# Performance work log

Hardware: AMD Instinct MI355X
Metric: run time of the kernel (lower is better)

## Reference

```python
import jax, jax.numpy as jnp
import numpy as np

N = 8192      # total nodes
B = 8         # graphs in batch
L = 1024      # nodes per graph (max_len)
E = 262144    # edges (before self loops)
IN = 64       # in_channels
H = 8         # heads
C = 32        # hidden_channels (per-head out dim)
D = H * C     # 256, d_model
DFF = 2048    # transformer FFN dim (torch default)
NEG = -1e9


def setup_inputs() -> dict:
    key = jax.random.key(0)
    ks = jax.random.split(key, 24)
    def p(i, shape):
        return jax.random.normal(ks[i], shape, jnp.float32) * 0.02
    x = jax.random.normal(ks[0], (N, IN), jnp.float32)
    src = jax.random.randint(ks[1], (E,), 0, N)
    dst = (src // L) * L + jax.random.randint(ks[2], (E,), 0, L)  # keep edges within a graph
    edge_index = jnp.stack([src, dst]).astype(jnp.int32)
    batch = (jnp.arange(N) // L).astype(jnp.int32)
    return dict(
        x=x, edge_index=edge_index, batch=batch,
        gat_W0=p(3, (D, IN)), gat_W12=p(4, (2, D, D)),
        gat_att_src=p(5, (3, H, C)), gat_att_dst=p(6, (3, H, C)), gat_bias=p(7, (3, D)),
        tf_qkv_w=p(8, (2, 3 * D, D)), tf_qkv_b=p(9, (2, 3 * D)),
        tf_out_w=p(10, (2, D, D)), tf_out_b=p(11, (2, D)),
        tf_ln1_w=jnp.ones((2, D)), tf_ln1_b=jnp.zeros((2, D)),
        tf_ln2_w=jnp.ones((2, D)), tf_ln2_b=jnp.zeros((2, D)),
        tf_ff1_w=p(12, (2, DFF, D)), tf_ff1_b=p(13, (2, DFF)),
        tf_ff2_w=p(14, (2, D, DFF)), tf_ff2_b=p(15, (2, D)),
        pred_w=p(16, (3, D)), pred_b=p(17, (3,)),
    )


def _gat(x, src, dst, W, att_s, att_d, bias):
    # PyG GATConv, concat=True, add_self_loops (appended in caller), eval (no dropout)
    h = (x @ W.T).reshape(-1, H, C)                       # [N,H,C]
    a_s = (h * att_s).sum(-1)                             # [N,H]
    a_d = (h * att_d).sum(-1)
    e = jax.nn.leaky_relu(a_s[src] + a_d[dst], 0.2)       # [E+N,H]
    m = jax.ops.segment_max(e, dst, num_segments=N)       # per-dst softmax
    e = jnp.exp(e - m[dst])
    s = jax.ops.segment_sum(e, dst, num_segments=N)
    alpha = e / s[dst]
    out = jax.ops.segment_sum(h[src] * alpha[..., None], dst, num_segments=N)
    return out.reshape(-1, D) + bias


def _ln(x, w, b):
    mu = x.mean(-1, keepdims=True)
    v = ((x - mu) ** 2).mean(-1, keepdims=True)
    return (x - mu) / jnp.sqrt(v + 1e-5) * w + b


def _tf_layer(x, mask, qkv_w, qkv_b, out_w, out_b, ln1w, ln1b, ln2w, ln2b, f1w, f1b, f2w, f2b):
    # torch TransformerEncoderLayer (post-LN, relu), key padding mask, eval mode
    qkv = x @ qkv_w.T + qkv_b                              # [B,L,3D]
    q, k, v = jnp.split(qkv, 3, -1)
    sh = lambda t: t.reshape(B, L, H, D // H)
    q, k, v = sh(q), sh(k), sh(v)
    sc = jnp.einsum('bqhd,bkhd->bhqk', q, k) * (1.0 / float(np.sqrt(D // H)))
    sc = jnp.where(mask[:, None, None, :], NEG, sc)
    a = jax.nn.softmax(sc, -1)
    o = jnp.einsum('bhqk,bkhd->bqhd', a, v).reshape(B, L, D)
    x = _ln(x + o @ out_w.T + out_b, ln1w, ln1b)
    f = jax.nn.relu(x @ f1w.T + f1b) @ f2w.T + f2b
    return _ln(x + f, ln2w, ln2b)


def reference(x, edge_index, batch, gat_W0, gat_W12, gat_att_src, gat_att_dst, gat_bias,
              tf_qkv_w, tf_qkv_b, tf_out_w, tf_out_b, tf_ln1_w, tf_ln1_b, tf_ln2_w, tf_ln2_b,
              tf_ff1_w, tf_ff1_b, tf_ff2_w, tf_ff2_b, pred_w, pred_b):
    loops = jnp.arange(N, dtype=edge_index.dtype)
    src = jnp.concatenate([edge_index[0], loops])
    dst = jnp.concatenate([edge_index[1], loops])
    h = jax.nn.relu(_gat(x, src, dst, gat_W0, gat_att_src[0], gat_att_dst[0], gat_bias[0]))
    for i in range(2):
        h = jax.nn.relu(_gat(h, src, dst, gat_W12[i], gat_att_src[i + 1], gat_att_dst[i + 1], gat_bias[i + 1]))
    # ragged -> padded [B, L, D] (vectorized scatter instead of python loop)
    seq_lens = jax.ops.segment_sum(jnp.ones(N, jnp.int32), batch, num_segments=B)
    starts = jnp.cumsum(seq_lens) - seq_lens
    pos = jnp.arange(N) - starts[batch]
    xp = jnp.zeros((B, L, D), h.dtype).at[batch, pos].set(h)
    mask = jnp.arange(L)[None, :] >= seq_lens[:, None]     # True = padded key
    for i in range(2):
        xp = _tf_layer(xp, mask, tf_qkv_w[i], tf_qkv_b[i], tf_out_w[i], tf_out_b[i],
                       tf_ln1_w[i], tf_ln1_b[i], tf_ln2_w[i], tf_ln2_b[i],
                       tf_ff1_w[i], tf_ff1_b[i], tf_ff2_w[i], tf_ff2_b[i])
    return xp @ pred_w.T + pred_b                          # [B,L,3]
```

## Files before the change

kernel.cpp:

```cpp
#include <hip/hip_runtime.h>
#include <hip/hip_bf16.h>

#define NN 8192
#define EE 262144
#define BB 8
#define LL 1024
#define HH 8
#define DD 256
#define DFFN 2048

typedef short s8v __attribute__((ext_vector_type(8)));
typedef float f32x4 __attribute__((ext_vector_type(4)));
typedef unsigned short ushort;

__device__ inline ushort f2bf(float f) {
    unsigned u = __float_as_uint(f);
    u = (u + 0x7fffu + ((u >> 16) & 1u)) >> 16;
    return (ushort)u;
}
__device__ inline float bf2f(ushort u) {
    return __uint_as_float(((unsigned)u) << 16);
}

template<bool BIAS, bool RELU, bool RES, bool WF, bool WB>
__global__ __launch_bounds__(256) void mgemm_kernel(
    const ushort* __restrict__ A, const ushort* __restrict__ W,
    const float* __restrict__ bias, const float* __restrict__ res,
    float* __restrict__ Cf, ushort* __restrict__ Cb, int M, int N, int K)
{
    __shared__ ushort As[128 * 64];
    __shared__ ushort Bs[128 * 64];
    int t = threadIdx.x;
    int l = t & 63;
    int quad = l >> 4, l15 = l & 15;
    int r7 = l15 & 7;
    int w = t >> 6;
    int wm = (w >> 1) * 64, wn = (w & 1) * 64;
    int m0 = blockIdx.x * 128, n0 = blockIdx.y * 128;

    f32x4 z = {0.f, 0.f, 0.f, 0.f};
    f32x4 acc[4][4];
#pragma unroll
    for (int i = 0; i < 4; ++i)
#pragma unroll
        for (int j = 0; j < 4; ++j) acc[i][j] = z;

    for (int k0 = 0; k0 < K; k0 += 64) {
#pragma unroll
        for (int i = 0; i < 4; ++i) {
            int chunk = i * 256 + t;
            int r = chunk >> 3, p = chunk & 7;
            int qs = (p ^ (r & 7)) * 8;
            __builtin_amdgcn_global_load_lds(
                (const __attribute__((address_space(1))) unsigned int*)
                    (A + (size_t)(m0 + r) * K + k0 + qs),
                (__attribute__((address_space(3))) unsigned int*)(As + chunk * 8), 16, 0, 0);
            __builtin_amdgcn_global_load_lds(
                (const __attribute__((address_space(1))) unsigned int*)
                    (W + (size_t)(n0 + r) * K + k0 + qs),
                (__attribute__((address_space(3))) unsigned int*)(Bs + chunk * 8), 16, 0, 0);
        }
        __syncthreads();
#pragma unroll
        for (int kk = 0; kk < 2; ++kk) {
            int off = ((kk * 4 + quad) ^ r7) * 8;
            s8v af[4], bfv[4];
#pragma unroll
            for (int i = 0; i < 4; ++i) {
                af[i]  = *(const s8v*)(As + (wm + i * 16 + l15) * 64 + off);
                bfv[i] = *(const s8v*)(Bs + (wn + i * 16 + l15) * 64 + off);
            }
#pragma unroll
            for (int mi = 0; mi < 4; ++mi)
#pragma unroll
                for (int ni = 0; ni < 4; ++ni)
                    acc[mi][ni] = __builtin_amdgcn_mfma_f32_16x16x32_bf16(
                        af[mi], bfv[ni], acc[mi][ni], 0, 0, 0);
        }
        __syncthreads();
    }

#pragma unroll
    for (int mi = 0; mi < 4; ++mi) {
#pragma unroll
        for (int ni = 0; ni < 4; ++ni) {
            int n = n0 + wn + ni * 16 + l15;
#pragma unroll
            for (int r = 0; r < 4; ++r) {
                int m = m0 + wm + mi * 16 + quad * 4 + r;
                float v = acc[mi][ni][r];
                if (BIAS) v += bias[n];
                if (RES)  v += res[(size_t)m * N + n];
                if (RELU) v = fmaxf(v, 0.f);
                if (WF) Cf[(size_t)m * N + n] = v;
                if (WB) Cb[(size_t)m * N + n] = f2bf(v);
            }
        }
    }
}

template<bool ASD>
__global__ __launch_bounds__(256) void mgemm64_kernel(
    const ushort* __restrict__ A, const ushort* __restrict__ W,
    ushort* __restrict__ Cb,
    const float* __restrict__ atts, const float* __restrict__ attd,
    float* __restrict__ a_s, float* __restrict__ a_d, int M, int N, int K)
{
    __shared__ ushort As[64 * 64];
    __shared__ ushort Bs[64 * 64];
    int t = threadIdx.x;
    int l = t & 63;
    int quad = l >> 4, l15 = l & 15;
    int r7 = l15 & 7;
    int w = t >> 6;
    int wm = (w >> 1) * 32, wn = (w & 1) * 32;
    int m0 = blockIdx.x * 64, n0 = blockIdx.y * 64;

    f32x4 z = {0.f, 0.f, 0.f, 0.f};
    f32x4 acc[2][2];
#pragma unroll
    for (int i = 0; i < 2; ++i)
#pragma unroll
        for (int j = 0; j < 2; ++j) acc[i][j] = z;

    for (int k0 = 0; k0 < K; k0 += 64) {
#pragma unroll
        for (int i = 0; i < 2; ++i) {
            int chunk = i * 256 + t;
            int r = chunk >> 3, p = chunk & 7;
            int qs = (p ^ (r & 7)) * 8;
            __builtin_amdgcn_global_load_lds(
                (const __attribute__((address_space(1))) unsigned int*)
                    (A + (size_t)(m0 + r) * K + k0 + qs),
                (__attribute__((address_space(3))) unsigned int*)(As + chunk * 8), 16, 0, 0);
            __builtin_amdgcn_global_load_lds(
                (const __attribute__((address_space(1))) unsigned int*)
                    (W + (size_t)(n0 + r) * K + k0 + qs),
                (__attribute__((address_space(3))) unsigned int*)(Bs + chunk * 8), 16, 0, 0);
        }
        __syncthreads();
#pragma unroll
        for (int kk = 0; kk < 2; ++kk) {
            s8v af[2], bfv[2];
            int off = ((kk * 4 + quad) ^ r7) * 8;
#pragma unroll
            for (int i = 0; i < 2; ++i) {
                af[i]  = *(const s8v*)(As + (wm + i * 16 + l15) * 64 + off);
                bfv[i] = *(const s8v*)(Bs + (wn + i * 16 + l15) * 64 + off);
            }
#pragma unroll
            for (int mi = 0; mi < 2; ++mi)
#pragma unroll
                for (int ni = 0; ni < 2; ++ni)
                    acc[mi][ni] = __builtin_amdgcn_mfma_f32_16x16x32_bf16(
                        af[mi], bfv[ni], acc[mi][ni], 0, 0, 0);
        }
        __syncthreads();
    }

#pragma unroll
    for (int mi = 0; mi < 2; ++mi) {
#pragma unroll
        for (int ni = 0; ni < 2; ++ni) {
            int n = n0 + wn + ni * 16 + l15;
#pragma unroll
            for (int r = 0; r < 4; ++r) {
                int m = m0 + wm + mi * 16 + quad * 4 + r;
                Cb[(size_t)m * N + n] = f2bf(acc[mi][ni][r]);
            }
        }
    }

    if (ASD) {
        int head = ((n0 + wn) >> 5) & 7;
        float as0 = atts[head * 32 + l15];
        float as1 = atts[head * 32 + 16 + l15];
        float ad0 = attd[head * 32 + l15];
        float ad1 = attd[head * 32 + 16 + l15];
#pragma unroll
        for (int mi = 0; mi < 2; ++mi)
#pragma unroll
            for (int r = 0; r < 4; ++r) {
                float sp = acc[mi][0][r] * as0 + acc[mi][1][r] * as1;
                float dp = acc[mi][0][r] * ad0 + acc[mi][1][r] * ad1;
#pragma unroll
                for (int off = 1; off < 16; off <<= 1) {
                    sp += __shfl_xor(sp, off);
                    dp += __shfl_xor(dp, off);
                }
                if (l15 == 0) {
                    int m = m0 + wm + mi * 16 + quad * 4 + r;
                    a_s[m * 8 + head] = sp;
                    a_d[m * 8 + head] = dp;
                }
            }
    }
}

__global__ __launch_bounds__(256) void gemm0_scatter_kernel(
    const ushort* __restrict__ A, const ushort* __restrict__ W,
    ushort* __restrict__ Cb,
    const float* __restrict__ atts, const float* __restrict__ attd,
    float* __restrict__ a_s, float* __restrict__ a_d,
    const int* __restrict__ ei, int* __restrict__ deg, int* __restrict__ col)
{
    __shared__ ushort As[64 * 64];
    __shared__ ushort Bs[64 * 64];
    int t = threadIdx.x;

    if (blockIdx.x >= 512) {
        int e = (blockIdx.x - 512) * 256 + t;
        if (e < EE + NN) {
            int s, d;
            if (e < EE) { s = ei[e]; d = ei[EE + e]; } else { s = e - EE; d = s; }
            int slot = atomicAdd(&deg[d], 1);
            col[(d << 7) + slot] = s;
        }
        return;
    }

    int l = t & 63;
    int quad = l >> 4, l15 = l & 15;
    int r7 = l15 & 7;
    int w = t >> 6;
    int wm = (w >> 1) * 32, wn = (w & 1) * 32;
    int m0 = (blockIdx.x & 127) * 64, n0 = (blockIdx.x >> 7) * 64;
    const int K = 64;

    f32x4 z = {0.f, 0.f, 0.f, 0.f};
    f32x4 acc[2][2];
#pragma unroll
    for (int i = 0; i < 2; ++i)
#pragma unroll
        for (int j = 0; j < 2; ++j) acc[i][j] = z;

#pragma unroll
    for (int i = 0; i < 2; ++i) {
        int chunk = i * 256 + t;
        int r = chunk >> 3, p = chunk & 7;
        int qs = (p ^ (r & 7)) * 8;
        __builtin_amdgcn_global_load_lds(
            (const __attribute__((address_space(1))) unsigned int*)
                (A + (size_t)(m0 + r) * K + qs),
            (__attribute__((address_space(3))) unsigned int*)(As + chunk * 8), 16, 0, 0);
        __builtin_amdgcn_global_load_lds(
            (const __attribute__((address_space(1))) unsigned int*)
                (W + (size_t)(n0 + r) * K + qs),
            (__attribute__((address_space(3))) unsigned int*)(Bs + chunk * 8), 16, 0, 0);
    }
    __syncthreads();
#pragma unroll
    for (int kk = 0; kk < 2; ++kk) {
        s8v af[2], bfv[2];
        int off = ((kk * 4 + quad) ^ r7) * 8;
#pragma unroll
        for (int i = 0; i < 2; ++i) {
            af[i]  = *(const s8v*)(As + (wm + i * 16 + l15) * 64 + off);
            bfv[i] = *(const s8v*)(Bs + (wn + i * 16 + l15) * 64 + off);
        }
#pragma unroll
        for (int mi = 0; mi < 2; ++mi)
#pragma unroll
            for (int ni = 0; ni < 2; ++ni)
                acc[mi][ni] = __builtin_amdgcn_mfma_f32_16x16x32_bf16(
                    af[mi], bfv[ni], acc[mi][ni], 0, 0, 0);
    }

#pragma unroll
    for (int mi = 0; mi < 2; ++mi) {
#pragma unroll
        for (int ni = 0; ni < 2; ++ni) {
            int n = n0 + wn + ni * 16 + l15;
#pragma unroll
            for (int r = 0; r < 4; ++r) {
                int m = m0 + wm + mi * 16 + quad * 4 + r;
                Cb[(size_t)m * DD + n] = f2bf(acc[mi][ni][r]);
            }
        }
    }

    {
        int head = ((n0 + wn) >> 5) & 7;
        float as0 = atts[head * 32 + l15];
        float as1 = atts[head * 32 + 16 + l15];
        float ad0 = attd[head * 32 + l15];
        float ad1 = attd[head * 32 + 16 + l15];
#pragma unroll
        for (int mi = 0; mi < 2; ++mi)
#pragma unroll
            for (int r = 0; r < 4; ++r) {
                float sp = acc[mi][0][r] * as0 + acc[mi][1][r] * as1;
                float dp = acc[mi][0][r] * ad0 + acc[mi][1][r] * ad1;
#pragma unroll
                for (int off = 1; off < 16; off <<= 1) {
                    sp += __shfl_xor(sp, off);
                    dp += __shfl_xor(dp, off);
                }
                if (l15 == 0) {
                    int m = m0 + wm + mi * 16 + quad * 4 + r;
                    a_s[m * 8 + head] = sp;
                    a_d[m * 8 + head] = dp;
                }
            }
    }
}

template<bool PRED>
__global__ __launch_bounds__(256) void mgemm_ln_kernel(
    const ushort* __restrict__ A, const ushort* __restrict__ W,
    const float* __restrict__ bias, const float* __restrict__ res,
    const float* __restrict__ lnw, const float* __restrict__ lnbb,
    float* __restrict__ Xf, ushort* __restrict__ Xb,
    const float* __restrict__ pw, const float* __restrict__ pb,
    float* __restrict__ pout, int M, int K)
{
    __shared__ ushort As[16 * 64];
    __shared__ ushort Bs[256 * 64];
    __shared__ float red[2][4][16];
    __shared__ float predred[4][16][3];

    int t = threadIdx.x;
    int l = t & 63;
    int quad = l >> 4, l15 = l & 15;
    int r7 = l15 & 7;
    int w = t >> 6;
    int m0 = blockIdx.x * 16;
    int n0w = w * 64;

    f32x4 z = {0.f, 0.f, 0.f, 0.f};
    f32x4 acc[4];
#pragma unroll
    for (int i = 0; i < 4; ++i) acc[i] = z;

    for (int k0 = 0; k0 < K; k0 += 64) {
#pragma unroll
        for (int i = 0; i < 8; ++i) {
            int chunk = i * 256 + t;
            int r = chunk >> 3, p = chunk & 7;
            int qs = (p ^ (r & 7)) * 8;
            __builtin_amdgcn_global_load_lds(
                (const __attribute__((address_space(1))) unsigned int*)
                    (W + (size_t)r * K + k0 + qs),
                (__attribute__((address_space(3))) unsigned int*)(Bs + chunk * 8), 16, 0, 0);
        }
        if (t < 128) {
            int r = t >> 3, p = t & 7;
            int qs = (p ^ (r & 7)) * 8;
            __builtin_amdgcn_global_load_lds(
                (const __attribute__((address_space(1))) unsigned int*)
                    (A + (size_t)(m0 + r) * K + k0 + qs),
                (__attribute__((address_space(3))) unsigned int*)(As + t * 8), 16, 0, 0);
        }
        __syncthreads();
#pragma unroll
        for (int kk = 0; kk < 2; ++kk) {
            int off = ((kk * 4 + quad) ^ r7) * 8;
            s8v af = *(const s8v*)(As + l15 * 64 + off);
#pragma unroll
            for (int ni = 0; ni < 4; ++ni) {
                s8v bfv = *(const s8v*)(Bs + (n0w + ni * 16 + l15) * 64 + off);
                acc[ni] = __builtin_amdgcn_mfma_f32_16x16x32_bf16(af, bfv, acc[ni], 0, 0, 0);
            }
        }
        __syncthreads();
    }

    float v[4][4];
#pragma unroll
    for (int ni = 0; ni < 4; ++ni) {
        int n = n0w + ni * 16 + l15;
        float bi = bias[n];
#pragma unroll
        for (int r = 0; r < 4; ++r) {
            int m = m0 + quad * 4 + r;
            v[ni][r] = acc[ni][r] + bi + res[(size_t)m * DD + n];
        }
    }
    float s1[4], s2[4];
#pragma unroll
    for (int r = 0; r < 4; ++r) {
        s1[r] = 0.f; s2[r] = 0.f;
#pragma unroll
        for (int ni = 0; ni < 4; ++ni) { s1[r] += v[ni][r]; s2[r] += v[ni][r] * v[ni][r]; }
#pragma unroll
        for (int off = 1; off < 16; off <<= 1) {
            s1[r] += __shfl_xor(s1[r], off);
            s2[r] += __shfl_xor(s2[r], off);
        }
    }
    if (l15 == 0)
#pragma unroll
        for (int r = 0; r < 4; ++r) {
            red[0][w][quad * 4 + r] = s1[r];
            red[1][w][quad * 4 + r] = s2[r];
        }
    __syncthreads();
    float mu[4], rstd[4];
#pragma unroll
    for (int r = 0; r < 4; ++r) {
        int row = quad * 4 + r;
        float S1 = red[0][0][row] + red[0][1][row] + red[0][2][row] + red[0][3][row];
        float S2 = red[1][0][row] + red[1][1][row] + red[1][2][row] + red[1][3][row];
        mu[r] = S1 * (1.f / 256.f);
        float var = S2 * (1.f / 256.f) - mu[r] * mu[r];
        rstd[r] = rsqrtf(fmaxf(var, 0.f) + 1e-5f);
    }

    float ov[4][4];
#pragma unroll
    for (int ni = 0; ni < 4; ++ni) {
        int n = n0w + ni * 16 + l15;
        float wl = lnw[n], bl = lnbb[n];
#pragma unroll
        for (int r = 0; r < 4; ++r)
            ov[ni][r] = (v[ni][r] - mu[r]) * rstd[r] * wl + bl;
    }

    if (PRED) {
        float ps[3][4] = {};
#pragma unroll
        for (int ni = 0; ni < 4; ++ni) {
            int n = n0w + ni * 16 + l15;
            float w0 = pw[n], w1 = pw[DD + n], w2 = pw[2 * DD + n];
#pragma unroll
            for (int r = 0; r < 4; ++r) {
                ps[0][r] += ov[ni][r] * w0;
                ps[1][r] += ov[ni][r] * w1;
                ps[2][r] += ov[ni][r] * w2;
            }
        }
#pragma unroll
        for (int o3 = 0; o3 < 3; ++o3)
#pragma unroll
            for (int r = 0; r < 4; ++r)
#pragma unroll
                for (int off = 1; off < 16; off <<= 1)
                    ps[o3][r] += __shfl_xor(ps[o3][r], off);
        if (l15 == 0)
#pragma unroll
            for (int o3 = 0; o3 < 3; ++o3)
#pragma unroll
                for (int r = 0; r < 4; ++r)
                    predred[w][quad * 4 + r][o3] = ps[o3][r];
        __syncthreads();
        if (t < 48) {
            int row = t / 3, o3 = t % 3;
            float s = predred[0][row][o3] + predred[1][row][o3]
                    + predred[2][row][o3] + predred[3][row][o3] + pb[o3];
            pout[(size_t)(m0 + row) * 3 + o3] = s;
        }
    } else {
#pragma unroll
        for (int ni = 0; ni < 4; ++ni) {
            int n = n0w + ni * 16 + l15;
#pragma unroll
            for (int r = 0; r < 4; ++r) {
                int m = m0 + quad * 4 + r;
                Xf[(size_t)m * DD + n] = ov[ni][r];
                Xb[(size_t)m * DD + n] = f2bf(ov[ni][r]);
            }
        }
    }
}

__global__ __launch_bounds__(256) void mgemm_qkv_kernel(
    const ushort* __restrict__ A, const ushort* __restrict__ W,
    const float* __restrict__ bias,
    ushort* __restrict__ Qb, ushort* __restrict__ Kb, ushort* __restrict__ Vt,
    int M, int K)
{
    __shared__ ushort As[64 * 64];
    __shared__ ushort Bs[64 * 64];
    int t = threadIdx.x;
    int l = t & 63;
    int quad = l >> 4, l15 = l & 15;
    int r7 = l15 & 7;
    int w = t >> 6;
    int wm = (w >> 1) * 32, wn = (w & 1) * 32;
    int m0 = blockIdx.x * 64, n0 = blockIdx.y * 64;

    f32x4 z = {0.f, 0.f, 0.f, 0.f};
    f32x4 acc[2][2];
#pragma unroll
    for (int i = 0; i < 2; ++i)
#pragma unroll
        for (int j = 0; j < 2; ++j) acc[i][j] = z;

    for (int k0 = 0; k0 < K; k0 += 64) {
#pragma unroll
        for (int i = 0; i < 2; ++i) {
            int chunk = i * 256 + t;
            int r = chunk >> 3, p = chunk & 7;
            int qs = (p ^ (r & 7)) * 8;
            __builtin_amdgcn_global_load_lds(
                (const __attribute__((address_space(1))) unsigned int*)
                    (A + (size_t)(m0 + r) * K + k0 + qs),
                (__attribute__((address_space(3))) unsigned int*)(As + chunk * 8), 16, 0, 0);
            __builtin_amdgcn_global_load_lds(
                (const __attribute__((address_space(1))) unsigned int*)
                    (W + (size_t)(n0 + r) * K + k0 + qs),
                (__attribute__((address_space(3))) unsigned int*)(Bs + chunk * 8), 16, 0, 0);
        }
        __syncthreads();
#pragma unroll
        for (int kk = 0; kk < 2; ++kk) {
            s8v af[2], bfv[2];
            int off = ((kk * 4 + quad) ^ r7) * 8;
#pragma unroll
            for (int i = 0; i < 2; ++i) {
                af[i]  = *(const s8v*)(As + (wm + i * 16 + l15) * 64 + off);
                bfv[i] = *(const s8v*)(Bs + (wn + i * 16 + l15) * 64 + off);
            }
#pragma unroll
            for (int mi = 0; mi < 2; ++mi)
#pragma unroll
                for (int ni = 0; ni < 2; ++ni)
                    acc[mi][ni] = __builtin_amdgcn_mfma_f32_16x16x32_bf16(
                        af[mi], bfv[ni], acc[mi][ni], 0, 0, 0);
        }
        __syncthreads();
    }

#pragma unroll
    for (int mi = 0; mi < 2; ++mi) {
#pragma unroll
        for (int ni = 0; ni < 2; ++ni) {
            int n = n0 + wn + ni * 16 + l15;
            int sec = n >> 8, hc = n & 255;
            int hh = hc >> 5, c = hc & 31;
            float bv = bias[n];
#pragma unroll
            for (int r = 0; r < 4; ++r) {
                int m = m0 + wm + mi * 16 + quad * 4 + r;
                float v = acc[mi][ni][r] + bv;
                int b = m >> 10, ll2 = m & 1023;
                int bh = b * 8 + hh;
                if (sec == 0)
                    Qb[(size_t)bh * 32768 + ll2 * 32 + c] = f2bf(v * 0.17677669529663687f);
                else if (sec == 1)
                    Kb[(size_t)bh * 32768 + ll2 * 32 + c] = f2bf(v);
                else
                    Vt[(size_t)bh * 32768 + c * 1024 + ll2] = f2bf(v);
            }
        }
    }
}

__global__ __launch_bounds__(256) void castall_kernel(
    const float* __restrict__ W0, const float* __restrict__ W12,
    const float* __restrict__ qkvw, const float* __restrict__ outw,
    const float* __restrict__ f1w, const float* __restrict__ f2w,
    const float* __restrict__ x,
    ushort* __restrict__ W0b, ushort* __restrict__ W12b,
    ushort* __restrict__ qkvb, ushort* __restrict__ outb,
    ushort* __restrict__ f1b, ushort* __restrict__ f2b,
    ushort* __restrict__ xb, int* __restrict__ deg)
{
    int tid = blockIdx.x * 256 + threadIdx.x;
    if (tid < 2048) *(int4*)(deg + tid * 4) = make_int4(0, 0, 0, 0);
    int e = tid * 4;
    if (e >= 3293184) return;
    const float* s; ushort* d; int off;
    if (e < 16384)        { s = W0;   d = W0b;  off = e; }
    else if (e < 147456)  { s = W12;  d = W12b; off = e - 16384; }
    else if (e < 540672)  { s = qkvw; d = qkvb; off = e - 147456; }
    else if (e < 671744)  { s = outw; d = outb; off = e - 540672; }
    else if (e < 1720320) { s = f1w;  d = f1b;  off = e - 671744; }
    else if (e < 2768896) { s = f2w;  d = f2b;  off = e - 1720320; }
    else                  { s = x;    d = xb;   off = e - 2768896; }
    float4 v = *(const float4*)(s + off);
    d[off + 0] = f2bf(v.x); d[off + 1] = f2bf(v.y);
    d[off + 2] = f2bf(v.z); d[off + 3] = f2bf(v.w);
}

template<bool WF>
__global__ __launch_bounds__(256) void gat_agg_kernel(
    const ushort* __restrict__ hlinb, const float* __restrict__ a_s,
    const float* __restrict__ a_d, const int* __restrict__ deg,
    const int* __restrict__ col, const float* __restrict__ bias,
    float* __restrict__ out, ushort* __restrict__ outb)
{
    int wid = threadIdx.x >> 6, lane = threadIdx.x & 63;
    int dst = blockIdx.x * 4 + wid;
    int start = dst << 7;
    int end = start + deg[dst];
    int myh = lane >> 3;
    float adh = a_d[(size_t)dst * HH + myh];

    float a0 = 0.f, a1 = 0.f, a2 = 0.f, a3 = 0.f, den = 0.f;
    int e = start;
    for (; e + 4 <= end; e += 4) {
        int s0 = col[e], s1 = col[e + 1], s2 = col[e + 2], s3 = col[e + 3];
        float v0 = a_s[(size_t)s0 * HH + myh] + adh;
        float v1 = a_s[(size_t)s1 * HH + myh] + adh;
        float v2 = a_s[(size_t)s2 * HH + myh] + adh;
        float v3 = a_s[(size_t)s3 * HH + myh] + adh;
        v0 = v0 > 0.f ? v0 : 0.2f * v0;
        v1 = v1 > 0.f ? v1 : 0.2f * v1;
        v2 = v2 > 0.f ? v2 : 0.2f * v2;
        v3 = v3 > 0.f ? v3 : 0.2f * v3;
        float p0 = __expf(v0), p1 = __expf(v1), p2 = __expf(v2), p3 = __expf(v3);
        den += p0 + p1 + p2 + p3;
        uint2 h0 = *(const uint2*)(hlinb + (size_t)s0 * DD + lane * 4);
        uint2 h1 = *(const uint2*)(hlinb + (size_t)s1 * DD + lane * 4);
        uint2 h2 = *(const uint2*)(hlinb + (size_t)s2 * DD + lane * 4);
        uint2 h3 = *(const uint2*)(hlinb + (size_t)s3 * DD + lane * 4);
        a0 += p0 * bf2f((ushort)(h0.x & 0xffff)) + p1 * bf2f((ushort)(h1.x & 0xffff))
            + p2 * bf2f((ushort)(h2.x & 0xffff)) + p3 * bf2f((ushort)(h3.x & 0xffff));
        a1 += p0 * bf2f((ushort)(h0.x >> 16)) + p1 * bf2f((ushort)(h1.x >> 16))
            + p2 * bf2f((ushort)(h2.x >> 16)) + p3 * bf2f((ushort)(h3.x >> 16));
        a2 += p0 * bf2f((ushort)(h0.y & 0xffff)) + p1 * bf2f((ushort)(h1.y & 0xffff))
            + p2 * bf2f((ushort)(h2.y & 0xffff)) + p3 * bf2f((ushort)(h3.y & 0xffff));
        a3 += p0 * bf2f((ushort)(h0.y >> 16)) + p1 * bf2f((ushort)(h1.y >> 16))
            + p2 * bf2f((ushort)(h2.y >> 16)) + p3 * bf2f((ushort)(h3.y >> 16));
    }
    for (; e < end; ++e) {
        int s = col[e];
        float v = a_s[(size_t)s * HH + myh] + adh;
        v = v > 0.f ? v : 0.2f * v;
        float p = __expf(v);
        den += p;
        uint2 hv = *(const uint2*)(hlinb + (size_t)s * DD + lane * 4);
        a0 += p * bf2f((ushort)(hv.x & 0xffff));
        a1 += p * bf2f((ushort)(hv.x >> 16));
        a2 += p * bf2f((ushort)(hv.y & 0xffff));
        a3 += p * bf2f((ushort)(hv.y >> 16));
    }
    float inv = 1.f / den;
    float4 bv = *(const float4*)(bias + lane * 4);
    float r0 = fmaxf(a0 * inv + bv.x, 0.f);
    float r1 = fmaxf(a1 * inv + bv.y, 0.f);
    float r2 = fmaxf(a2 * inv + bv.z, 0.f);
    float r3 = fmaxf(a3 * inv + bv.w, 0.f);
    if (WF) {
        float* op = out + (size_t)dst * DD + lane * 4;
        op[0] = r0; op[1] = r1; op[2] = r2; op[3] = r3;
    }
    ushort* ob = outb + (size_t)dst * DD + lane * 4;
    ob[0] = f2bf(r0); ob[1] = f2bf(r1); ob[2] = f2bf(r2); ob[3] = f2bf(r3);
}

__global__ __launch_bounds__(256, 2) void attn_flash_kernel(
    const ushort* __restrict__ Qb, const ushort* __restrict__ Kb,
    const ushort* __restrict__ Vt, ushort* __restrict__ outb)
{
    __shared__ ushort Ks[2][128 * 32];
    __shared__ ushort Vs[2][32 * 128];
    __shared__ ushort pw[4][32][132];

    int t = threadIdx.x;
    int w = t >> 6, lane = t & 63;
    int quad = lane >> 4, l15 = lane & 15;
    int kq = (quad ^ ((l15 >> 1) & 3)) * 8;
    int bh = blockIdx.y;
    int q0 = blockIdx.x * 128 + w * 32;
    int b = bh >> 3, h = bh & 7;

    const ushort* qbase = Qb + (size_t)bh * 32768;
    const ushort* kbase = Kb + (size_t)bh * 32768;
    const ushort* vbase = Vt + (size_t)bh * 32768;

    s8v aq0 = *(const s8v*)(qbase + (q0 + l15) * 32 + quad * 8);
    s8v aq1 = *(const s8v*)(qbase + (q0 + 16 + l15) * 32 + quad * 8);

    int i0 = t, i1 = 256 + t;
    int kr0 = i0 >> 2, kcs0 = (((i0 & 3)) ^ ((kr0 >> 1) & 3)) * 8;
    int kr1 = i1 >> 2, kcs1 = (((i1 & 3)) ^ ((kr1 >> 1) & 3)) * 8;
    int vr0 = i0 >> 4, vcs0 = ((i0 & 15) ^ (vr0 & 15)) * 8;
    int vr1 = i1 >> 4, vcs1 = ((i1 & 15) ^ (vr1 & 15)) * 8;

#define STAGE(ch, bf)                                                          \
    {                                                                          \
        int j0 = (ch) * 128;                                                   \
        __builtin_amdgcn_global_load_lds(                                      \
            (const __attribute__((address_space(1))) unsigned int*)            \
                (kbase + (size_t)(j0 + kr0) * 32 + kcs0),                      \
            (__attribute__((address_space(3))) unsigned int*)(Ks[bf] + i0 * 8), 16, 0, 0); \
        __builtin_amdgcn_global_load_lds(                                      \
            (const __attribute__((address_space(1))) unsigned int*)            \
                (kbase + (size_t)(j0 + kr1) * 32 + kcs1),                      \
            (__attribute__((address_space(3))) unsigned int*)(Ks[bf] + i1 * 8), 16, 0, 0); \
        __builtin_amdgcn_global_load_lds(                                      \
            (const __attribute__((address_space(1))) unsigned int*)            \
                (vbase + (size_t)vr0 * 1024 + j0 + vcs0),                      \
            (__attribute__((address_space(3))) unsigned int*)(Vs[bf] + i0 * 8), 16, 0, 0); \
        __builtin_amdgcn_global_load_lds(                                      \
            (const __attribute__((address_space(1))) unsigned int*)            \
                (vbase + (size_t)vr1 * 1024 + j0 + vcs1),                      \
            (__attribute__((address_space(3))) unsigned int*)(Vs[bf] + i1 * 8), 16, 0, 0); \
    }

    f32x4 z = {0.f, 0.f, 0.f, 0.f};
    f32x4 o00 = z, o01 = z, o10 = z, o11 = z;
    float lden0[4] = {0.f, 0.f, 0.f, 0.f};
    float lden1[4] = {0.f, 0.f, 0.f, 0.f};

    STAGE(0, 0);
    for (int ch = 0; ch < 8; ++ch) {
        int bf = ch & 1;
        __syncthreads();
        if (ch < 7) STAGE(ch + 1, bf ^ 1);

        f32x4 s0[8], s1[8];
#pragma unroll
        for (int kk = 0; kk < 8; ++kk) {
            s8v bk = *(const s8v*)(Ks[bf] + (kk * 16 + l15) * 32 + kq);
            s0[kk] = __builtin_amdgcn_mfma_f32_16x16x32_bf16(aq0, bk, z, 0, 0, 0);
            s1[kk] = __builtin_amdgcn_mfma_f32_16x16x32_bf16(aq1, bk, z, 0, 0, 0);
        }

        float cs0[4] = {0.f, 0.f, 0.f, 0.f};
        float cs1[4] = {0.f, 0.f, 0.f, 0.f};
#pragma unroll
        for (int kk = 0; kk < 8; ++kk) {
#pragma unroll
            for (int r = 0; r < 4; ++r) {
                float p0 = __expf(s0[kk][r]);
                float p1 = __expf(s1[kk][r]);
                cs0[r] += p0;
                cs1[r] += p1;
                pw[w][quad * 4 + r][kk * 16 + l15]      = f2bf(p0);
                pw[w][16 + quad * 4 + r][kk * 16 + l15] = f2bf(p1);
            }
        }
#pragma unroll
        for (int r = 0; r < 4; ++r) {
#pragma unroll
            for (int off = 1; off < 16; off <<= 1) {
                cs0[r] += __shfl_xor(cs0[r], off);
                cs1[r] += __shfl_xor(cs1[r], off);
            }
            lden0[r] += cs0[r];
            lden1[r] += cs1[r];
        }

#pragma unroll
        for (int kk = 0; kk < 4; ++kk) {
            s8v ap0 = *(const s8v*)(&pw[w][l15][kk * 32 + quad * 8]);
            s8v ap1 = *(const s8v*)(&pw[w][16 + l15][kk * 32 + quad * 8]);
            int c0 = ((kk * 4 + quad) ^ l15) * 8;
            s8v b0 = *(const s8v*)(Vs[bf] + (size_t)l15 * 128 + c0);
            s8v b1 = *(const s8v*)(Vs[bf] + (size_t)(16 + l15) * 128 + c0);
            o00 = __builtin_amdgcn_mfma_f32_16x16x32_bf16(ap0, b0, o00, 0, 0, 0);
            o01 = __builtin_amdgcn_mfma_f32_16x16x32_bf16(ap0, b1, o01, 0, 0, 0);
            o10 = __builtin_amdgcn_mfma_f32_16x16x32_bf16(ap1, b0, o10, 0, 0, 0);
            o11 = __builtin_amdgcn_mfma_f32_16x16x32_bf16(ap1, b1, o11, 0, 0, 0);
        }
    }
#undef STAGE

#pragma unroll
    for (int r = 0; r < 4; ++r) {
        int row0 = q0 + quad * 4 + r;
        int row1 = row0 + 16;
        float i0v = 1.f / lden0[r];
        float i1v = 1.f / lden1[r];
        outb[(size_t)(b * 1024 + row0) * 256 + h * 32 + l15]      = f2bf(o00[r] * i0v);
        outb[(size_t)(b * 1024 + row0) * 256 + h * 32 + 16 + l15] = f2bf(o01[r] * i0v);
        outb[(size_t)(b * 1024 + row1) * 256 + h * 32 + l15]      = f2bf(o10[r] * i1v);
        outb[(size_t)(b * 1024 + row1) * 256 + h * 32 + 16 + l15] = f2bf(o11[r] * i1v);
    }
}

extern "C" void kernel_launch(void* const* d_in, const int* in_sizes, int n_in,
                              void* d_out, int out_size, void* d_ws, size_t ws_size,
                              hipStream_t stream)
{
    const float* x        = (const float*)d_in[0];
    const int*   ei       = (const int*)d_in[1];
    const float* gat_W0   = (const float*)d_in[3];
    const float* gat_W12  = (const float*)d_in[4];
    const float* att_src  = (const float*)d_in[5];
    const float* att_dst  = (const float*)d_in[6];
    const float* gat_bias = (const float*)d_in[7];
    const float* qkv_w    = (const float*)d_in[8];
    const float* qkv_b    = (const float*)d_in[9];
    const float* out_w    = (const float*)d_in[10];
    const float* out_b    = (const float*)d_in[11];
    const float* ln1_w    = (const float*)d_in[12];
    const float* ln1_b    = (const float*)d_in[13];
    const float* ln2_w    = (const float*)d_in[14];
    const float* ln2_b    = (const float*)d_in[15];
    const float* ff1_w    = (const float*)d_in[16];
    const float* ff1_b    = (const float*)d_in[17];
    const float* ff2_w    = (const float*)d_in[18];
    const float* ff2_b    = (const float*)d_in[19];
    const float* pred_w   = (const float*)d_in[20];
    const float* pred_b   = (const float*)d_in[21];
    float* outp = (float*)d_out;

    float* ws   = (float*)d_ws;
    float* hA   = ws;
    float* hB   = ws + 2097152;
    ushort* ffb  = (ushort*)(ws + 4194304);
    ushort* Qb   = (ushort*)(ws + 12582912);
    ushort* Kb   = (ushort*)(ws + 13631488);
    ushort* Vt   = (ushort*)(ws + 14680064);
    ushort* attnb= (ushort*)(ws + 15728640);
    ushort* lnb  = (ushort*)(ws + 16777216);
    ushort* hBb  = (ushort*)(ws + 17825792);
    ushort* xb   = (ushort*)(ws + 18874368);
    ushort* wbase= (ushort*)(ws + 19136512);
    ushort* W0b    = wbase;
    ushort* W12b   = wbase + 16384;
    ushort* qkv_wb = wbase + 147456;
    ushort* out_wb = wbase + 540672;
    ushort* ff1_wb = wbase + 671744;
    ushort* ff2_wb = wbase + 1720320;
    float* a_s  = ws + 20520960;
    float* a_d  = ws + 20586496;
    int*   deg  = (int*)(ws + 20652032);
    ushort* hAb    = (ushort*)(ws + 21000192);
    int*   col  = (int*)(ws + 30437376);

    castall_kernel<<<3216, 256, 0, stream>>>(
        gat_W0, gat_W12, qkv_w, out_w, ff1_w, ff2_w, x,
        W0b, W12b, qkv_wb, out_wb, ff1_wb, ff2_wb, xb, deg);

    gemm0_scatter_kernel<<<1568, 256, 0, stream>>>(
        xb, W0b, hAb, att_src, att_dst, a_s, a_d, ei, deg, col);
    gat_agg_kernel<false><<<2048, 256, 0, stream>>>(
        hAb, a_s, a_d, deg, col, gat_bias, nullptr, hBb);

    for (int l = 0; l < 2; ++l) {
        mgemm64_kernel<true><<<dim3(128, 4), 256, 0, stream>>>(
            hBb, W12b + (size_t)l * DD * DD, hAb,
            att_src + (l + 1) * 256, att_dst + (l + 1) * 256, a_s, a_d, NN, DD, DD);
        if (l == 0)
            gat_agg_kernel<false><<<2048, 256, 0, stream>>>(
                hAb, a_s, a_d, deg, col, gat_bias + 256, nullptr, hBb);
        else
            gat_agg_kernel<true><<<2048, 256, 0, stream>>>(
                hAb, a_s, a_d, deg, col, gat_bias + 512, hB, hBb);
    }

    for (int l = 0; l < 2; ++l) {
        mgemm_qkv_kernel<<<dim3(128, 12), 256, 0, stream>>>(
            hBb, qkv_wb + (size_t)l * 768 * DD, qkv_b + l * 768, Qb, Kb, Vt, NN, DD);
        attn_flash_kernel<<<dim3(8, 64), 256, 0, stream>>>(Qb, Kb, Vt, attnb);
        mgemm_ln_kernel<false><<<512, 256, 0, stream>>>(
            attnb, out_wb + (size_t)l * DD * DD, out_b + l * DD, hB,
            ln1_w + l * DD, ln1_b + l * DD, hA, lnb,
            nullptr, nullptr, nullptr, NN, DD);
        mgemm_kernel<true, true, false, false, true><<<dim3(64, 16), 256, 0, stream>>>(
            lnb, ff1_wb + (size_t)l * DFFN * DD, ff1_b + l * DFFN, nullptr,
            nullptr, ffb, NN, DFFN, DD);
        if (l == 0) {
            mgemm_ln_kernel<false><<<512, 256, 0, stream>>>(
                ffb, ff2_wb, ff2_b, hA,
                ln2_w, ln2_b, hB, hBb,
                nullptr, nullptr, nullptr, NN, DFFN);
        } else {
            mgemm_ln_kernel<true><<<512, 256, 0, stream>>>(
                ffb, ff2_wb + (size_t)DD * DFFN, ff2_b + DD, hA,
                ln2_w + DD, ln2_b + DD, nullptr, nullptr,
                pred_w, pred_b, outp, NN, DFFN);
        }
    }
}
```

Baseline: 387.0 us.

## Widen FFN1 GEMM tile, double LN-GEMM rows per block, compute softmax denominators via MFMA

Result: no change. 385.6 us (-0.4%).

```diff
diff --git a/kernel.cpp b/kernel.cpp
--- a/kernel.cpp
+++ b/kernel.cpp
@@ -22,28 +22,27 @@
     return __uint_as_float(((unsigned)u) << 16);
 }
 
-template<bool BIAS, bool RELU, bool RES, bool WF, bool WB>
-__global__ __launch_bounds__(256) void mgemm_kernel(
+__global__ __launch_bounds__(256, 2) void mgemm_wide_kernel(
     const ushort* __restrict__ A, const ushort* __restrict__ W,
-    const float* __restrict__ bias, const float* __restrict__ res,
-    float* __restrict__ Cf, ushort* __restrict__ Cb, int M, int N, int K)
+    const float* __restrict__ bias, ushort* __restrict__ Cb,
+    int M, int N, int K)
 {
     __shared__ ushort As[128 * 64];
-    __shared__ ushort Bs[128 * 64];
+    __shared__ ushort Bs[256 * 64];
     int t = threadIdx.x;
     int l = t & 63;
     int quad = l >> 4, l15 = l & 15;
     int r7 = l15 & 7;
     int w = t >> 6;
-    int wm = (w >> 1) * 64, wn = (w & 1) * 64;
-    int m0 = blockIdx.x * 128, n0 = blockIdx.y * 128;
+    int wm = (w >> 1) * 64, wn = (w & 1) * 128;
+    int m0 = blockIdx.x * 128, n0 = blockIdx.y * 256;
 
     f32x4 z = {0.f, 0.f, 0.f, 0.f};
-    f32x4 acc[4][4];
+    f32x4 acc[4][8];
 #pragma unroll
     for (int i = 0; i < 4; ++i)
 #pragma unroll
-        for (int j = 0; j < 4; ++j) acc[i][j] = z;
+        for (int j = 0; j < 8; ++j) acc[i][j] = z;
 
     for (int k0 = 0; k0 < K; k0 += 64) {
 #pragma unroll
@@ -55,6 +54,12 @@
                 (const __attribute__((address_space(1))) unsigned int*)
                     (A + (size_t)(m0 + r) * K + k0 + qs),
                 (__attribute__((address_space(3))) unsigned int*)(As + chunk * 8), 16, 0, 0);
+        }
+#pragma unroll
+        for (int i = 0; i < 8; ++i) {
+            int chunk = i * 256 + t;
+            int r = chunk >> 3, p = chunk & 7;
+            int qs = (p ^ (r & 7)) * 8;
             __builtin_amdgcn_global_load_lds(
                 (const __attribute__((address_space(1))) unsigned int*)
                     (W + (size_t)(n0 + r) * K + k0 + qs),
@@ -64,36 +69,33 @@
 #pragma unroll
         for (int kk = 0; kk < 2; ++kk) {
             int off = ((kk * 4 + quad) ^ r7) * 8;
-            s8v af[4], bfv[4];
-#pragma unroll
-            for (int i = 0; i < 4; ++i) {
-                af[i]  = *(const s8v*)(As + (wm + i * 16 + l15) * 64 + off);
-                bfv[i] = *(const s8v*)(Bs + (wn + i * 16 + l15) * 64 + off);
-            }
-#pragma unroll
-            for (int mi = 0; mi < 4; ++mi)
-#pragma unroll
-                for (int ni = 0; ni < 4; ++ni)
+            s8v af[4];
+#pragma unroll
+            for (int i = 0; i < 4; ++i)
+                af[i] = *(const s8v*)(As + (wm + i * 16 + l15) * 64 + off);
+#pragma unroll
+            for (int ni = 0; ni < 8; ++ni) {
+                s8v bfv = *(const s8v*)(Bs + (wn + ni * 16 + l15) * 64 + off);
+#pragma unroll
+                for (int mi = 0; mi < 4; ++mi)
                     acc[mi][ni] = __builtin_amdgcn_mfma_f32_16x16x32_bf16(
-                        af[mi], bfv[ni], acc[mi][ni], 0, 0, 0);
-        }
-        __syncthreads();
-    }
-
-#pragma unroll
-    for (int mi = 0; mi < 4; ++mi) {
-#pragma unroll
-        for (int ni = 0; ni < 4; ++ni) {
-            int n = n0 + wn + ni * 16 + l15;
+                        af[mi], bfv, acc[mi][ni], 0, 0, 0);
+            }
+        }
+        __syncthreads();
+    }
+
+#pragma unroll
+    for (int ni = 0; ni < 8; ++ni) {
+        int n = n0 + wn + ni * 16 + l15;
+        float bi = bias[n];
+#pragma unroll
+        for (int mi = 0; mi < 4; ++mi) {
 #pragma unroll
             for (int r = 0; r < 4; ++r) {
                 int m = m0 + wm + mi * 16 + quad * 4 + r;
-                float v = acc[mi][ni][r];
-                if (BIAS) v += bias[n];
-                if (RES)  v += res[(size_t)m * N + n];
-                if (RELU) v = fmaxf(v, 0.f);
-                if (WF) Cf[(size_t)m * N + n] = v;
-                if (WB) Cb[(size_t)m * N + n] = f2bf(v);
+                float v = fmaxf(acc[mi][ni][r] + bi, 0.f);
+                Cb[(size_t)m * N + n] = f2bf(v);
             }
         }
     }
@@ -306,7 +308,7 @@
 }
 
 template<bool PRED>
-__global__ __launch_bounds__(256) void mgemm_ln_kernel(
+__global__ __launch_bounds__(512) void mgemm_ln_kernel(
     const ushort* __restrict__ A, const ushort* __restrict__ W,
     const float* __restrict__ bias, const float* __restrict__ res,
     const float* __restrict__ lnw, const float* __restrict__ lnbb,
@@ -314,18 +316,20 @@
     const float* __restrict__ pw, const float* __restrict__ pb,
     float* __restrict__ pout, int M, int K)
 {
-    __shared__ ushort As[16 * 64];
+    __shared__ ushort As[32 * 64];
     __shared__ ushort Bs[256 * 64];
-    __shared__ float red[2][4][16];
-    __shared__ float predred[4][16][3];
+    __shared__ float red[2][4][32];
+    __shared__ float predred[4][32][3];
 
     int t = threadIdx.x;
     int l = t & 63;
     int quad = l >> 4, l15 = l & 15;
     int r7 = l15 & 7;
     int w = t >> 6;
-    int m0 = blockIdx.x * 16;
-    int n0w = w * 64;
+    int mh = w >> 2;
+    int cw = w & 3;
+    int n0w = cw * 64;
+    int m0 = blockIdx.x * 32;
 
     f32x4 z = {0.f, 0.f, 0.f, 0.f};
     f32x4 acc[4];
@@ -334,8 +338,8 @@
 
     for (int k0 = 0; k0 < K; k0 += 64) {
 #pragma unroll
-        for (int i = 0; i < 8; ++i) {
-            int chunk = i * 256 + t;
+        for (int i = 0; i < 4; ++i) {
+            int chunk = i * 512 + t;
             int r = chunk >> 3, p = chunk & 7;
             int qs = (p ^ (r & 7)) * 8;
             __builtin_amdgcn_global_load_lds(
@@ -343,7 +347,7 @@
                     (W + (size_t)r * K + k0 + qs),
                 (__attribute__((address_space(3))) unsigned int*)(Bs + chunk * 8), 16, 0, 0);
         }
-        if (t < 128) {
+        if (t < 256) {
             int r = t >> 3, p = t & 7;
             int qs = (p ^ (r & 7)) * 8;
             __builtin_amdgcn_global_load_lds(
@@ -355,7 +359,7 @@
 #pragma unroll
         for (int kk = 0; kk < 2; ++kk) {
             int off = ((kk * 4 + quad) ^ r7) * 8;
-            s8v af = *(const s8v*)(As + l15 * 64 + off);
+            s8v af = *(const s8v*)(As + (mh * 16 + l15) * 64 + off);
 #pragma unroll
             for (int ni = 0; ni < 4; ++ni) {
                 s8v bfv = *(const s8v*)(Bs + (n0w + ni * 16 + l15) * 64 + off);
@@ -372,7 +376,7 @@
         float bi = bias[n];
 #pragma unroll
         for (int r = 0; r < 4; ++r) {
-            int m = m0 + quad * 4 + r;
+            int m = m0 + mh * 16 + quad * 4 + r;
             v[ni][r] = acc[ni][r] + bi + res[(size_t)m * DD + n];
         }
     }
@@ -391,14 +395,15 @@
     if (l15 == 0)
 #pragma unroll
         for (int r = 0; r < 4; ++r) {
-            red[0][w][quad * 4 + r] = s1[r];
-            red[1][w][quad * 4 + r] = s2[r];
+            int row = mh * 16 + quad * 4 + r;
+            red[0][cw][row] = s1[r];
+            red[1][cw][row] = s2[r];
         }
     __syncthreads();
     float mu[4], rstd[4];
 #pragma unroll
     for (int r = 0; r < 4; ++r) {
-        int row = quad * 4 + r;
+        int row = mh * 16 + quad * 4 + r;
         float S1 = red[0][0][row] + red[0][1][row] + red[0][2][row] + red[0][3][row];
         float S2 = red[1][0][row] + red[1][1][row] + red[1][2][row] + red[1][3][row];
         mu[r] = S1 * (1.f / 256.f);
@@ -441,9 +446,9 @@
             for (int o3 = 0; o3 < 3; ++o3)
 #pragma unroll
                 for (int r = 0; r < 4; ++r)
-                    predred[w][quad * 4 + r][o3] = ps[o3][r];
-        __syncthreads();
-        if (t < 48) {
+                    predred[cw][mh * 16 + quad * 4 + r][o3] = ps[o3][r];
+        __syncthreads();
+        if (t < 96) {
             int row = t / 3, o3 = t % 3;
             float s = predred[0][row][o3] + predred[1][row][o3]
                     + predred[2][row][o3] + predred[3][row][o3] + pb[o3];
@@ -455,7 +460,7 @@
             int n = n0w + ni * 16 + l15;
 #pragma unroll
             for (int r = 0; r < 4; ++r) {
-                int m = m0 + quad * 4 + r;
+                int m = m0 + mh * 16 + quad * 4 + r;
                 Xf[(size_t)m * DD + n] = ov[ni][r];
                 Xb[(size_t)m * DD + n] = f2bf(ov[ni][r]);
             }
@@ -663,6 +668,10 @@
     s8v aq0 = *(const s8v*)(qbase + (q0 + l15) * 32 + quad * 8);
     s8v aq1 = *(const s8v*)(qbase + (q0 + 16 + l15) * 32 + quad * 8);
 
+    s8v vone;
+#pragma unroll
+    for (int i = 0; i < 8; ++i) vone[i] = (short)0x3F80;
+
     int i0 = t, i1 = 256 + t;
     int kr0 = i0 >> 2, kcs0 = (((i0 & 3)) ^ ((kr0 >> 1) & 3)) * 8;
     int kr1 = i1 >> 2, kcs1 = (((i1 & 3)) ^ ((kr1 >> 1) & 3)) * 8;
@@ -692,8 +701,7 @@
 
     f32x4 z = {0.f, 0.f, 0.f, 0.f};
     f32x4 o00 = z, o01 = z, o10 = z, o11 = z;
-    float lden0[4] = {0.f, 0.f, 0.f, 0.f};
-    float lden1[4] = {0.f, 0.f, 0.f, 0.f};
+    f32x4 od0 = z, od1 = z;
 
     STAGE(0, 0);
     for (int ch = 0; ch < 8; ++ch) {
@@ -709,29 +717,15 @@
             s1[kk] = __builtin_amdgcn_mfma_f32_16x16x32_bf16(aq1, bk, z, 0, 0, 0);
         }
 
-        float cs0[4] = {0.f, 0.f, 0.f, 0.f};
-        float cs1[4] = {0.f, 0.f, 0.f, 0.f};
 #pragma unroll
         for (int kk = 0; kk < 8; ++kk) {
 #pragma unroll
             for (int r = 0; r < 4; ++r) {
                 float p0 = __expf(s0[kk][r]);
                 float p1 = __expf(s1[kk][r]);
-                cs0[r] += p0;
-                cs1[r] += p1;
                 pw[w][quad * 4 + r][kk * 16 + l15]      = f2bf(p0);
                 pw[w][16 + quad * 4 + r][kk * 16 + l15] = f2bf(p1);
             }
-        }
-#pragma unroll
-        for (int r = 0; r < 4; ++r) {
-#pragma unroll
-            for (int off = 1; off < 16; off <<= 1) {
-                cs0[r] += __shfl_xor(cs0[r], off);
-                cs1[r] += __shfl_xor(cs1[r], off);
-            }
-            lden0[r] += cs0[r];
-            lden1[r] += cs1[r];
         }
 
 #pragma unroll
@@ -745,6 +739,8 @@
             o01 = __builtin_amdgcn_mfma_f32_16x16x32_bf16(ap0, b1, o01, 0, 0, 0);
             o10 = __builtin_amdgcn_mfma_f32_16x16x32_bf16(ap1, b0, o10, 0, 0, 0);
             o11 = __builtin_amdgcn_mfma_f32_16x16x32_bf16(ap1, b1, o11, 0, 0, 0);
+            od0 = __builtin_amdgcn_mfma_f32_16x16x32_bf16(ap0, vone, od0, 0, 0, 0);
+            od1 = __builtin_amdgcn_mfma_f32_16x16x32_bf16(ap1, vone, od1, 0, 0, 0);
         }
     }
 #undef STAGE
@@ -753,8 +749,8 @@
     for (int r = 0; r < 4; ++r) {
         int row0 = q0 + quad * 4 + r;
         int row1 = row0 + 16;
-        float i0v = 1.f / lden0[r];
-        float i1v = 1.f / lden1[r];
+        float i0v = 1.f / od0[r];
+        float i1v = 1.f / od1[r];
         outb[(size_t)(b * 1024 + row0) * 256 + h * 32 + l15]      = f2bf(o00[r] * i0v);
         outb[(size_t)(b * 1024 + row0) * 256 + h * 32 + 16 + l15] = f2bf(o01[r] * i0v);
         outb[(size_t)(b * 1024 + row1) * 256 + h * 32 + l15]      = f2bf(o10[r] * i1v);
@@ -838,20 +834,19 @@
         mgemm_qkv_kernel<<<dim3(128, 12), 256, 0, stream>>>(
             hBb, qkv_wb + (size_t)l * 768 * DD, qkv_b + l * 768, Qb, Kb, Vt, NN, DD);
         attn_flash_kernel<<<dim3(8, 64), 256, 0, stream>>>(Qb, Kb, Vt, attnb);
-        mgemm_ln_kernel<false><<<512, 256, 0, stream>>>(
+        mgemm_ln_kernel<false><<<256, 512, 0, stream>>>(
             attnb, out_wb + (size_t)l * DD * DD, out_b + l * DD, hB,
             ln1_w + l * DD, ln1_b + l * DD, hA, lnb,
             nullptr, nullptr, nullptr, NN, DD);
-        mgemm_kernel<true, true, false, false, true><<<dim3(64, 16), 256, 0, stream>>>(
-            lnb, ff1_wb + (size_t)l * DFFN * DD, ff1_b + l * DFFN, nullptr,
-            nullptr, ffb, NN, DFFN, DD);
+        mgemm_wide_kernel<<<dim3(64, 8), 256, 0, stream>>>(
+            lnb, ff1_wb + (size_t)l * DFFN * DD, ff1_b + l * DFFN, ffb, NN, DFFN, DD);
         if (l == 0) {
-            mgemm_ln_kernel<false><<<512, 256, 0, stream>>>(
+            mgemm_ln_kernel<false><<<256, 512, 0, stream>>>(
                 ffb, ff2_wb, ff2_b, hA,
                 ln2_w, ln2_b, hB, hBb,
                 nullptr, nullptr, nullptr, NN, DFFN);
         } else {
-            mgemm_ln_kernel<true><<<512, 256, 0, stream>>>(
+            mgemm_ln_kernel<true><<<256, 512, 0, stream>>>(
                 ffb, ff2_wb + (size_t)DD * DFFN, ff2_b + DD, hA,
                 ln2_w + DD, ln2_b + DD, nullptr, nullptr,
                 pred_w, pred_b, outp, NN, DFFN);
```
